# Kernel tuning notes

Hardware: AMD Instinct MI355X
Metric: run time of the kernel (lower is better)

The kernel has to match this reference:

```python
import jax, jax.numpy as jnp
import numpy as np

B, P, K = 8, 1024, 20  # clouds, points per cloud, kNN neighbors
OUT = 40
EPS = 1e-5


def leaky(x):
    return jnp.where(x >= 0, x, 0.2 * x)


def batch_norm(h, gamma, beta):
    mu = jnp.mean(h, axis=0)
    var = jnp.var(h, axis=0)
    return (h - mu) * jax.lax.rsqrt(var + EPS) * gamma + beta


def edge_conv(x, W, b, k):
    # x: [B,P,C]. Dynamic kNN in feature space (self included, as torch_cluster knn),
    # edge feature nn([x_i, x_j - x_i]) (single plain Linear per PyG MLP plain_last),
    # then max-aggregation over the k neighbors.
    sq = jnp.sum(x * x, axis=-1)                                  # [B,P]
    d = sq[:, :, None] + sq[:, None, :] - 2.0 * jnp.einsum('bpc,bqc->bpq', x, x)
    idx = jax.lax.top_k(-d, k)[1]                                  # [B,P,k]
    xj = jax.vmap(lambda xc, ic: xc[ic])(x, idx)                   # [B,P,k,C]
    xi = jnp.broadcast_to(x[:, :, None, :], xj.shape)
    e = jnp.concatenate([xi, xj - xi], axis=-1)                    # [B,P,k,2C]
    h = jnp.einsum('bpke,ec->bpkc', e, W) + b
    return jnp.max(h, axis=2)                                      # [B,P,Cout]


def setup_inputs() -> dict:
    key = jax.random.key(0)
    ks = jax.random.split(key, 16)
    s = 0.1
    pos = jax.random.normal(ks[0], (B * P, 3), dtype=jnp.float32)
    batch = jnp.repeat(jnp.arange(B, dtype=jnp.int32), P)
    return {
        'pos': pos, 'batch': batch,
        'W1': jax.random.normal(ks[1], (6, 64), jnp.float32) * s,    'b1': jnp.zeros((64,), jnp.float32),
        'W2': jax.random.normal(ks[2], (128, 64), jnp.float32) * s,  'b2': jnp.zeros((64,), jnp.float32),
        'W3': jax.random.normal(ks[3], (128, 128), jnp.float32) * s, 'b3': jnp.zeros((128,), jnp.float32),
        'W4': jax.random.normal(ks[4], (256, 256), jnp.float32) * s, 'b4': jnp.zeros((256,), jnp.float32),
        'Wm': jax.random.normal(ks[5], (512, 1024), jnp.float32) * s, 'bm': jnp.zeros((1024,), jnp.float32),
        'Wa': jax.random.normal(ks[6], (2048, 512), jnp.float32) * s, 'ba': jnp.zeros((512,), jnp.float32),
        'ga': jnp.ones((512,), jnp.float32),  'bea': jnp.zeros((512,), jnp.float32),
        'Wb': jax.random.normal(ks[7], (512, 256), jnp.float32) * s, 'bb': jnp.zeros((256,), jnp.float32),
        'gb': jnp.ones((256,), jnp.float32),  'beb': jnp.zeros((256,), jnp.float32),
        'Wc': jax.random.normal(ks[8], (256, OUT), jnp.float32) * s, 'bc': jnp.zeros((OUT,), jnp.float32),
    }


def reference(pos, batch, W1, b1, W2, b2, W3, b3, W4, b4, Wm, bm,
              Wa, ba, ga, bea, Wb, bb, gb, beb, Wc, bc):
    # batch ids are contiguous with P points per cloud -> reshape to [B,P,.]
    x = pos.reshape(B, P, 3)
    x1 = edge_conv(x, W1, b1, K)    # [B,P,64]
    x2 = edge_conv(x1, W2, b2, K)   # [B,P,64]
    x3 = edge_conv(x2, W3, b3, K)   # [B,P,128]
    x4 = edge_conv(x3, W4, b4, K)   # [B,P,256]
    cat = jnp.concatenate([x1, x2, x3, x4], axis=-1)  # [B,P,512]
    out = cat @ Wm + bm                                # [B,P,1024] (plain Linear)
    gmax = jnp.max(out, axis=1)                        # global_max_pool  [B,1024]
    gmean = jnp.mean(out, axis=1)                      # global_mean_pool [B,1024]
    h = jnp.concatenate([gmax, gmean], axis=-1)        # [B,2048]
    h = leaky(batch_norm(h @ Wa + ba, ga, bea))        # dropout = identity (eval)
    h = leaky(batch_norm(h @ Wb + bb, gb, beb))
    return h @ Wc + bc                                 # [B,40]
```

## Files before the change

### kernel.cpp

```cpp
#include <hip/hip_runtime.h>
#include <hip/hip_bf16.h>

#define NB 8
#define NP 1024
#define NPTS (NB * NP)
#define KNN 20

using bf16x8 = __attribute__((ext_vector_type(8))) short;
using f32x4 = __attribute__((ext_vector_type(4))) float;

static __device__ __forceinline__ unsigned long long umin64(unsigned long long a,
                                                            unsigned long long b) {
    return a < b ? a : b;
}

static __device__ __forceinline__ void split_bf16(float v, unsigned short& h,
                                                  unsigned short& l) {
    __hip_bfloat16 hb = __float2bfloat16(v);
    float hf = __bfloat162float(hb);
    __hip_bfloat16 lb = __float2bfloat16(v - hf);
    h = *(unsigned short*)&hb;
    l = *(unsigned short*)&lb;
}

static __device__ __forceinline__ unsigned long long wave_bitonic_sort(
        unsigned long long v, int lane) {
#pragma unroll
    for (int k = 2; k <= 64; k <<= 1) {
#pragma unroll
        for (int j = k >> 1; j > 0; j >>= 1) {
            unsigned long long o = __shfl_xor(v, j, 64);
            bool tmin = (((lane & k) == 0) == ((lane & j) == 0));
            bool lt = v < o;
            v = (lt == tmin) ? v : o;
        }
    }
    return v;
}

static __device__ __forceinline__ void topk20_wave(unsigned long long k[16], int lane,
                                                   int* __restrict__ out) {
    for (int r = 0; r < KNN; ++r) {
        unsigned long long m = k[0];
#pragma unroll
        for (int j = 1; j < 16; ++j)
            if ((unsigned)(k[j] >> 32) < (unsigned)(m >> 32)) m = k[j];
#pragma unroll
        for (int s = 1; s < 64; s <<= 1) {
            unsigned long long o = __shfl_xor(m, s, 64);
            m = umin64(m, o);
        }
        if (lane == 0) out[r] = (int)(m & 0xffffffffu);
        if (r == KNN - 1) break;
        unsigned mlo = (unsigned)m;
#pragma unroll
        for (int j = 0; j < 16; ++j)
            if ((unsigned)k[j] == mlo) k[j] = ~0ull;
    }
}

static __device__ __forceinline__ void topk20_fast(unsigned long long k[16], int lane,
                                                   unsigned long long* __restrict__ cand,
                                                   int* __restrict__ out) {
    unsigned long long lm = k[0];
#pragma unroll
    for (int j = 1; j < 16; ++j) lm = umin64(lm, k[j]);
    unsigned long long s = wave_bitonic_sort(lm, lane);
    unsigned long long T = __shfl(s, 19, 64);

    int base = 0;
#pragma unroll
    for (int j = 0; j < 16; ++j) {
        bool sel = (k[j] <= T);
        unsigned long long mask = __ballot(sel);
        if (sel) {
            int pos = base + (int)__popcll(mask & ((1ull << lane) - 1ull));
            if (pos < 64) cand[pos] = k[j];
        }
        base += (int)__popcll(mask);
    }
    if (base <= 64) {
        unsigned long long v = (lane < base) ? cand[lane] : ~0ull;
        v = wave_bitonic_sort(v, lane);
        if (lane < KNN) out[lane] = (int)(v & 0xffffffffu);
    } else {
        topk20_wave(k, lane, out);
    }
}

__global__ __launch_bounds__(256) void knn3_kernel(const float* __restrict__ x,
                                                   int* __restrict__ idx) {
    const int w = threadIdx.x >> 6, lane = threadIdx.x & 63;
    const int p = blockIdx.x * 4 + w;
    const int b = p >> 10, pr = p & 1023;
    const int tid = threadIdx.x;
    __shared__ float sx[3][1024];
    __shared__ float ssq[1024];
    __shared__ unsigned long long cand[4][64];
    const float* xb = x + (size_t)b * NP * 3;

    for (int t = tid; t < 1024; t += 256) {
        float vx = xb[t * 3 + 0], vy = xb[t * 3 + 1], vz = xb[t * 3 + 2];
        sx[0][t] = vx;
        sx[1][t] = vy;
        sx[2][t] = vz;
        ssq[t] = vx * vx + vy * vy + vz * vz;
    }
    __syncthreads();

    const float px = sx[0][pr], py = sx[1][pr], pz = sx[2][pr];
    const float sqp = ssq[pr];

    unsigned long long k[16];
#pragma unroll
    for (int j = 0; j < 16; ++j) {
        int q = j * 64 + lane;
        float dot = px * sx[0][q];
        dot += py * sx[1][q];
        dot += pz * sx[2][q];
        float d = sqp + ssq[q] - 2.0f * dot;
        unsigned u = __float_as_uint(d);
        u = (u & 0x80000000u) ? ~u : (u | 0x80000000u);
        k[j] = ((unsigned long long)u << 32) | (unsigned)q;
    }
    topk20_fast(k, lane, cand[w], idx + (size_t)p * KNN);
}

template <int C>
__global__ __launch_bounds__(256) void sqnorm_kernel(const float* __restrict__ x,
                                                     float* __restrict__ sqn) {
    int p = blockIdx.x * 256 + threadIdx.x;
    if (p < NPTS) {
        const float* xp = x + (size_t)p * C;
        float s = 0.f;
        for (int c = 0; c < C; ++c) s += xp[c] * xp[c];
        sqn[p] = s;
    }
}

template <int C>
__global__ __launch_bounds__(256) void convert_x_kernel(const float* __restrict__ x,
                                                        unsigned short* __restrict__ Xh,
                                                        unsigned short* __restrict__ Xl) {
    int g = blockIdx.x * 256 + threadIdx.x;
    int p = g & (NPTS - 1), ks = g >> 13;
    const float* src = x + (size_t)p * C + ks * 8;
    float4 v0 = ((const float4*)src)[0];
    float4 v1 = ((const float4*)src)[1];
    float v[8] = {v0.x, v0.y, v0.z, v0.w, v1.x, v1.y, v1.z, v1.w};
    unsigned short h[8], l[8];
#pragma unroll
    for (int j = 0; j < 8; ++j) split_bf16(v[j], h[j], l[j]);
    size_t ci = (size_t)ks * NPTS + p;
    uint4 hp, lp;
    hp.x = h[0] | ((unsigned)h[1] << 16);
    hp.y = h[2] | ((unsigned)h[3] << 16);
    hp.z = h[4] | ((unsigned)h[5] << 16);
    hp.w = h[6] | ((unsigned)h[7] << 16);
    lp.x = l[0] | ((unsigned)l[1] << 16);
    lp.y = l[2] | ((unsigned)l[3] << 16);
    lp.z = l[4] | ((unsigned)l[5] << 16);
    lp.w = l[6] | ((unsigned)l[7] << 16);
    ((uint4*)Xh)[ci] = hp;
    ((uint4*)Xl)[ci] = lp;
}

template <int Cin, int Cout>
__global__ __launch_bounds__(256) void convert_w_edge_kernel(
        const float* __restrict__ W, unsigned short* __restrict__ Wh,
        unsigned short* __restrict__ Wl) {
    constexpr int N2 = 2 * Cout;
    int g = blockIdx.x * 256 + threadIdx.x;
    if (g >= (Cin / 8) * N2) return;
    int n = g % N2, ks = g / N2;
    unsigned short h[8], l[8];
#pragma unroll
    for (int j = 0; j < 8; ++j) {
        int c = ks * 8 + j;
        float v;
        if (n < Cout)
            v = W[(size_t)c * Cout + n] - W[(size_t)(Cin + c) * Cout + n];
        else
            v = W[(size_t)(Cin + c) * Cout + (n - Cout)];
        split_bf16(v, h[j], l[j]);
    }
    size_t ci = (size_t)ks * N2 + n;
    uint4 hp, lp;
    hp.x = h[0] | ((unsigned)h[1] << 16);
    hp.y = h[2] | ((unsigned)h[3] << 16);
    hp.z = h[4] | ((unsigned)h[5] << 16);
    hp.w = h[6] | ((unsigned)h[7] << 16);
    lp.x = l[0] | ((unsigned)l[1] << 16);
    lp.y = l[2] | ((unsigned)l[3] << 16);
    lp.z = l[4] | ((unsigned)l[5] << 16);
    lp.w = l[6] | ((unsigned)l[7] << 16);
    ((uint4*)Wh)[ci] = hp;
    ((uint4*)Wl)[ci] = lp;
}

template <int C>
__global__ __launch_bounds__(256, 2) void knn_mfma_kernel(
        const unsigned short* __restrict__ Xhp, const unsigned short* __restrict__ Xlp,
        const float* __restrict__ sqn, int* __restrict__ idx) {
    constexpr int NCK = C / 32;
    const int bid = blockIdx.x;
    const int b = bid >> 6, rg = bid & 63;
    const int g0 = b * NP;
    const int p0 = rg * 16;
    const int tid = threadIdx.x;
    const int wid = tid >> 6, lane = tid & 63;
    const int fkb = lane >> 4, flm = lane & 15;

    __shared__ float sD[16][1028];
    __shared__ float sqa[16];
    __shared__ float sqb[1024];
    __shared__ unsigned long long cand[4][64];

    if (tid < 16) sqa[tid] = sqn[g0 + p0 + tid];
    for (int t = tid; t < 1024; t += 256) sqb[t] = sqn[g0 + t];
    __syncthreads();

    const uint4* Ah4 = (const uint4*)Xhp;
    const uint4* Al4 = (const uint4*)Xlp;

    uint4 fAh[NCK], fAl[NCK];
#pragma unroll
    for (int kk = 0; kk < NCK; ++kk) {
        size_t a = (size_t)(4 * kk + fkb) * NPTS + g0 + p0 + flm;
        fAh[kk] = Ah4[a];
        fAl[kk] = Al4[a];
    }

    const int r4 = fkb * 4, cc = flm;

#pragma unroll
    for (int t = 0; t < 2; ++t) {
        const int c0 = (wid + t * 4) * 128;
        f32x4 acc[8];
#pragma unroll
        for (int j = 0; j < 8; ++j) acc[j] = {0.f, 0.f, 0.f, 0.f};

#pragma unroll
        for (int kk = 0; kk < NCK; ++kk) {
            uint4 fBh[8], fBl[8];
#pragma unroll
            for (int j = 0; j < 8; ++j) {
                size_t bi = (size_t)(4 * kk + fkb) * NPTS + g0 + c0 + j * 16 + flm;
                fBh[j] = Ah4[bi];
                fBl[j] = Al4[bi];
            }
            bf16x8 ah = *(const bf16x8*)&fAh[kk];
            bf16x8 al = *(const bf16x8*)&fAl[kk];
#pragma unroll
            for (int j = 0; j < 8; ++j) {
                bf16x8 bh = *(const bf16x8*)&fBh[j];
                bf16x8 bl = *(const bf16x8*)&fBl[j];
                acc[j] = __builtin_amdgcn_mfma_f32_16x16x32_bf16(ah, bh, acc[j], 0, 0, 0);
                acc[j] = __builtin_amdgcn_mfma_f32_16x16x32_bf16(ah, bl, acc[j], 0, 0, 0);
                acc[j] = __builtin_amdgcn_mfma_f32_16x16x32_bf16(al, bh, acc[j], 0, 0, 0);
            }
        }

#pragma unroll
        for (int r = 0; r < 4; ++r) {
            int row = r4 + r;
            float sp = sqa[row];
#pragma unroll
            for (int j = 0; j < 8; ++j) {
                int col = c0 + j * 16 + cc;
                sD[row][col] = sp + sqb[col] - 2.0f * acc[j][r];
            }
        }
    }
    __syncthreads();

    for (int rr = 0; rr < 4; ++rr) {
        int row = wid * 4 + rr;
        unsigned long long k[16];
#pragma unroll
        for (int j = 0; j < 16; ++j) {
            int q = j * 64 + lane;
            float dv = sD[row][q];
            unsigned u = __float_as_uint(dv);
            u = (u & 0x80000000u) ? ~u : (u | 0x80000000u);
            k[j] = ((unsigned long long)u << 32) | (unsigned)q;
        }
        topk20_fast(k, lane, cand[wid], idx + (size_t)(g0 + p0 + row) * KNN);
        __builtin_amdgcn_s_barrier();
    }
}

template <int Cin, int Cout>
__global__ __launch_bounds__(256, 2) void edge_mfma_kernel(
        const unsigned short* __restrict__ Xhp, const unsigned short* __restrict__ Xlp,
        const unsigned short* __restrict__ Whp, const unsigned short* __restrict__ Wlp,
        const float* __restrict__ bias, float* __restrict__ AB) {
    constexpr int N2 = 2 * Cout;
    constexpr int NCK = Cin / 32;
    const int n0 = blockIdx.x * 128;
    const int p0 = blockIdx.y * 128;
    const int tid = threadIdx.x;
    const int wid = tid >> 6, lane = tid & 63;
    const int wm = (wid >> 1) * 64, wn = (wid & 1) * 64;

    __shared__ uint4 sAh[2][4][132], sAl[2][4][132], sBh[2][4][132], sBl[2][4][132];

    f32x4 acc[4][4];
#pragma unroll
    for (int i = 0; i < 4; ++i)
#pragma unroll
        for (int j = 0; j < 4; ++j) acc[i][j] = {0.f, 0.f, 0.f, 0.f};

    const uint4* Ah4 = (const uint4*)Xhp;
    const uint4* Al4 = (const uint4*)Xlp;
    const uint4* Wh4 = (const uint4*)Whp;
    const uint4* Wl4 = (const uint4*)Wlp;

    const int m0 = tid & 127, kb0 = tid >> 7;
    uint4 rAh0, rAl0, rBh0, rBl0, rAh1, rAl1, rBh1, rBl1;

#define EM_LOAD(ck)                                                     \
    {                                                                   \
        int ksb = (ck) * 4;                                             \
        size_t a0 = (size_t)(ksb + kb0) * NPTS + p0 + m0;               \
        size_t a1 = (size_t)(ksb + kb0 + 2) * NPTS + p0 + m0;           \
        size_t b0 = (size_t)(ksb + kb0) * N2 + n0 + m0;                 \
        size_t b1 = (size_t)(ksb + kb0 + 2) * N2 + n0 + m0;             \
        rAh0 = Ah4[a0]; rAl0 = Al4[a0];                                 \
        rAh1 = Ah4[a1]; rAl1 = Al4[a1];                                 \
        rBh0 = Wh4[b0]; rBl0 = Wl4[b0];                                 \
        rBh1 = Wh4[b1]; rBl1 = Wl4[b1];                                 \
    }

#define EM_WRITE(buf)                                                   \
    {                                                                   \
        sAh[buf][kb0][m0] = rAh0;  sAl[buf][kb0][m0] = rAl0;            \
        sAh[buf][kb0 + 2][m0] = rAh1;  sAl[buf][kb0 + 2][m0] = rAl1;    \
        sBh[buf][kb0][m0] = rBh0;  sBl[buf][kb0][m0] = rBl0;            \
        sBh[buf][kb0 + 2][m0] = rBh1;  sBl[buf][kb0 + 2][m0] = rBl1;    \
    }

    EM_LOAD(0);
    EM_WRITE(0);
    __syncthreads();

    const int fkb = lane >> 4, flm = lane & 15;

    for (int ck = 0; ck < NCK; ++ck) {
        const int buf = ck & 1;
        if (ck < NCK - 1) EM_LOAD(ck + 1);

        bf16x8 fAh[4], fAl[4], fBh[4], fBl[4];
#pragma unroll
        for (int i = 0; i < 4; ++i) {
            fAh[i] = *(const bf16x8*)&sAh[buf][fkb][wm + i * 16 + flm];
            fAl[i] = *(const bf16x8*)&sAl[buf][fkb][wm + i * 16 + flm];
            fBh[i] = *(const bf16x8*)&sBh[buf][fkb][wn + i * 16 + flm];
            fBl[i] = *(const bf16x8*)&sBl[buf][fkb][wn + i * 16 + flm];
        }
#pragma unroll
        for (int i = 0; i < 4; ++i)
#pragma unroll
            for (int j = 0; j < 4; ++j) {
                acc[i][j] = __builtin_amdgcn_mfma_f32_16x16x32_bf16(fAh[i], fBh[j],
                                                                    acc[i][j], 0, 0, 0);
                acc[i][j] = __builtin_amdgcn_mfma_f32_16x16x32_bf16(fAh[i], fBl[j],
                                                                    acc[i][j], 0, 0, 0);
                acc[i][j] = __builtin_amdgcn_mfma_f32_16x16x32_bf16(fAl[i], fBh[j],
                                                                    acc[i][j], 0, 0, 0);
            }

        if (ck < NCK - 1) EM_WRITE(buf ^ 1);
        __syncthreads();
    }

    const int r4 = (lane >> 4) * 4, cc = lane & 15;
    float bj[4];
#pragma unroll
    for (int j = 0; j < 4; ++j) {
        int cg = n0 + wn + j * 16 + cc;
        bj[j] = (cg < Cout) ? bias[cg] : 0.f;
    }
#pragma unroll
    for (int i = 0; i < 4; ++i) {
#pragma unroll
        for (int r = 0; r < 4; ++r) {
            int row = wm + i * 16 + r4 + r;
            float* orow = AB + (size_t)(p0 + row) * N2 + n0;
#pragma unroll
            for (int j = 0; j < 4; ++j)
                orow[wn + j * 16 + cc] = acc[i][j][r] + bj[j];
        }
    }
#undef EM_LOAD
#undef EM_WRITE
}

template <int Cin, int Cout>
__global__ __launch_bounds__(256) void edge_gemm_kernel(const float* __restrict__ x,
                                                        const float* __restrict__ W,
                                                        const float* __restrict__ bias,
                                                        float* __restrict__ AB) {
    constexpr int N2 = 2 * Cout;
    constexpr int BK = (Cin < 32) ? Cin : 32;
    const int n0 = blockIdx.x * 128;
    const int p0 = blockIdx.y * 64;
    const int tid = threadIdx.x;
    const int tx = tid & 15, ty = tid >> 4;

    __shared__ float sX[BK][68];
    __shared__ float sW[BK][132];

    float acc[4][8];
#pragma unroll
    for (int i = 0; i < 4; ++i)
#pragma unroll
        for (int j = 0; j < 8; ++j) acc[i][j] = 0.f;

    for (int k0 = 0; k0 < Cin; k0 += BK) {
        for (int t = tid; t < 64 * BK; t += 256) {
            int m = t / BK, c = t - m * BK;
            sX[c][m] = x[(size_t)(p0 + m) * Cin + c];
        }
        for (int t = tid; t < BK * 128; t += 256) {
            int c = t >> 7, n = t & 127;
            int nn = n0 + n;
            float w;
            if (nn < Cout)
                w = W[(size_t)(k0 + c) * Cout + nn] - W[(size_t)(Cin + k0 + c) * Cout + nn];
            else
                w = W[(size_t)(Cin + k0 + c) * Cout + (nn - Cout)];
            sW[c][n] = w;
        }
        __syncthreads();

#pragma unroll
        for (int c = 0; c < BK; ++c) {
            float4 a4 = *(const float4*)&sX[c][ty * 4];
            float4 w0 = *(const float4*)&sW[c][tx * 4];
            float4 w1 = *(const float4*)&sW[c][64 + tx * 4];
            float av[4] = {a4.x, a4.y, a4.z, a4.w};
#pragma unroll
            for (int i = 0; i < 4; ++i) {
                acc[i][0] += av[i] * w0.x;
                acc[i][1] += av[i] * w0.y;
                acc[i][2] += av[i] * w0.z;
                acc[i][3] += av[i] * w0.w;
                acc[i][4] += av[i] * w1.x;
                acc[i][5] += av[i] * w1.y;
                acc[i][6] += av[i] * w1.z;
                acc[i][7] += av[i] * w1.w;
            }
        }
        __syncthreads();
    }

    const bool aH0 = (n0 < Cout);
    const bool aH1 = (n0 + 64 < Cout);
    float4 z4 = {0.f, 0.f, 0.f, 0.f};
    float4 bb0 = aH0 ? *(const float4*)&bias[n0 + tx * 4] : z4;
    float4 bb1 = aH1 ? *(const float4*)&bias[n0 + 64 + tx * 4] : z4;

#pragma unroll
    for (int i = 0; i < 4; ++i) {
        float* orow = AB + (size_t)(p0 + ty * 4 + i) * N2 + n0;
        float4 o0, o1;
        o0.x = acc[i][0] + bb0.x;
        o0.y = acc[i][1] + bb0.y;
        o0.z = acc[i][2] + bb0.z;
        o0.w = acc[i][3] + bb0.w;
        o1.x = acc[i][4] + bb1.x;
        o1.y = acc[i][5] + bb1.y;
        o1.z = acc[i][6] + bb1.z;
        o1.w = acc[i][7] + bb1.w;
        *(float4*)&orow[tx * 4] = o0;
        *(float4*)&orow[64 + tx * 4] = o1;
    }
}

template <int Cout>
__global__ __launch_bounds__(256) void gather_max_kernel(const float* __restrict__ AB,
                                                         const int* __restrict__ idx,
                                                         float* __restrict__ y) {
    constexpr int N2 = 2 * Cout;
    constexpr int TPP = Cout / 4;
    constexpr int PPB = 256 / TPP;
    constexpr int RS = N2 / 4;
    const int pp = threadIdx.x / TPP;
    const int t = threadIdx.x % TPP;
    const int p = blockIdx.x * PPB + pp;
    const int base = p & ~(NP - 1);

    __shared__ int s_idx[PPB][KNN];
    for (int tt = threadIdx.x; tt < PPB * KNN; tt += 256) {
        int a = tt / KNN, r = tt - a * KNN;
        s_idx[a][r] = idx[(size_t)(blockIdx.x * PPB + a) * KNN + r];
    }
    __syncthreads();

    const float4* Brow = (const float4*)(AB + (size_t)base * N2 + Cout);

    int q0 = s_idx[pp][0];
    float4 m = Brow[(size_t)q0 * RS + t];
#pragma unroll
    for (int j = 1; j < KNN; ++j) {
        int q = s_idx[pp][j];
        float4 v = Brow[(size_t)q * RS + t];
        m.x = fmaxf(m.x, v.x);
        m.y = fmaxf(m.y, v.y);
        m.z = fmaxf(m.z, v.z);
        m.w = fmaxf(m.w, v.w);
    }
    float4 a = *(const float4*)(AB + (size_t)p * N2 + 4 * t);
    float4 o;
    o.x = a.x + m.x;
    o.y = a.y + m.y;
    o.z = a.z + m.z;
    o.w = a.w + m.w;
    *(float4*)(y + (size_t)p * Cout + 4 * t) = o;
}

__global__ __launch_bounds__(256) void convert_w_kernel(const float* __restrict__ Wm,
                                                        unsigned short* __restrict__ Wh,
                                                        unsigned short* __restrict__ Wl) {
    int g = blockIdx.x * 256 + threadIdx.x;
    int n = g & 1023, ks = g >> 10;
    unsigned short h[8], l[8];
#pragma unroll
    for (int j = 0; j < 8; ++j) {
        float v = Wm[(size_t)(ks * 8 + j) * 1024 + n];
        split_bf16(v, h[j], l[j]);
    }
    size_t ci = (size_t)ks * 1024 + n;
    uint4 hp, lp;
    hp.x = h[0] | ((unsigned)h[1] << 16);
    hp.y = h[2] | ((unsigned)h[3] << 16);
    hp.z = h[4] | ((unsigned)h[5] << 16);
    hp.w = h[6] | ((unsigned)h[7] << 16);
    lp.x = l[0] | ((unsigned)l[1] << 16);
    lp.y = l[2] | ((unsigned)l[3] << 16);
    lp.z = l[4] | ((unsigned)l[5] << 16);
    lp.w = l[6] | ((unsigned)l[7] << 16);
    ((uint4*)Wh)[ci] = hp;
    ((uint4*)Wl)[ci] = lp;
}

__global__ __launch_bounds__(256) void catmean_kernel(
        const float* __restrict__ x1, const float* __restrict__ x2,
        const float* __restrict__ x3, const float* __restrict__ x4,
        float* __restrict__ catmean) {
    const int n0 = blockIdx.x * 128;
    const int b = blockIdx.y;
    const int tid = threadIdx.x;
    const int col = n0 + (tid & 127);
    const int half = tid >> 7;
    __shared__ float sred[256];

    const float* src;
    int cw, coff;
    if (col < 64) { src = x1; cw = 64; coff = col; }
    else if (col < 128) { src = x2; cw = 64; coff = col - 64; }
    else if (col < 256) { src = x3; cw = 128; coff = col - 128; }
    else { src = x4; cw = 256; coff = col - 256; }

    float s = 0.f;
    const float* base = src + ((size_t)b * NP + half * 512) * cw + coff;
    for (int p = 0; p < 512; ++p) s += base[(size_t)p * cw];
    sred[tid] = s;
    __syncthreads();
    if (tid < 128)
        catmean[(size_t)b * 512 + col] = (sred[tid] + sred[tid + 128]) * (1.0f / 1024.0f);
}

__global__ __launch_bounds__(256) void gmean_kernel(const float* __restrict__ catmean,
                                                    const float* __restrict__ Wm,
                                                    const float* __restrict__ bm,
                                                    float* __restrict__ gmeanv) {
    const int n0 = blockIdx.x * 128;
    const int b = blockIdx.y;
    const int tid = threadIdx.x;
    const int cg = tid & 31, kp = tid >> 5;
    const int col = n0 + cg * 4;
    __shared__ float4 part[8][32];

    float4 acc = {0.f, 0.f, 0.f, 0.f};
    for (int k = kp * 64; k < kp * 64 + 64; ++k) {
        float g = catmean[(size_t)b * 512 + k];
        float4 w = *(const float4*)&Wm[(size_t)k * 1024 + col];
        acc.x += g * w.x;
        acc.y += g * w.y;
        acc.z += g * w.z;
        acc.w += g * w.w;
    }
    part[kp][cg] = acc;
    __syncthreads();
    if (tid < 32) {
        float4 s = part[0][tid];
#pragma unroll
        for (int z = 1; z < 8; ++z) {
            float4 p = part[z][tid];
            s.x += p.x; s.y += p.y; s.z += p.z; s.w += p.w;
        }
        float4 bb = *(const float4*)&bm[n0 + tid * 4];
        s.x += bb.x; s.y += bb.y; s.z += bb.z; s.w += bb.w;
        *(float4*)&gmeanv[(size_t)b * 1024 + n0 + tid * 4] = s;
    }
}

__global__ __launch_bounds__(256, 2) void gemm_cat_pool_kernel(
        const unsigned short* __restrict__ Ahp, const unsigned short* __restrict__ Alp,
        const unsigned short* __restrict__ Whp, const unsigned short* __restrict__ Wlp,
        float* __restrict__ pmax) {
    const int bid = blockIdx.x;
    const int xcd = bid & 7, pos = bid >> 3;
    const int nb = pos & 7, pb = (xcd << 3) | (pos >> 3);
    const int n0 = nb * 128, p0 = pb * 128;
    const int tid = threadIdx.x;
    const int wid = tid >> 6, lane = tid & 63;
    const int wm = (wid >> 1) * 64, wn = (wid & 1) * 64;

    __shared__ uint4 sAh[2][4][132], sAl[2][4][132], sBh[2][4][132], sBl[2][4][132];
    __shared__ float sMax[2][128];

    f32x4 acc[4][4];
#pragma unroll
    for (int i = 0; i < 4; ++i)
#pragma unroll
        for (int j = 0; j < 4; ++j) acc[i][j] = {0.f, 0.f, 0.f, 0.f};

    const uint4* Ah4 = (const uint4*)Ahp;
    const uint4* Al4 = (const uint4*)Alp;
    const uint4* Wh4 = (const uint4*)Whp;
    const uint4* Wl4 = (const uint4*)Wlp;

    const int m0 = tid & 127, kb0 = tid >> 7;
    uint4 rAh0, rAl0, rBh0, rBl0, rAh1, rAl1, rBh1, rBl1;

#define MP_LOAD(ck)                                                     \
    {                                                                   \
        int ksb = (ck) * 4;                                             \
        size_t a0 = (size_t)(ksb + kb0) * 8192 + p0 + m0;               \
        size_t a1 = (size_t)(ksb + kb0 + 2) * 8192 + p0 + m0;           \
        size_t b0 = (size_t)(ksb + kb0) * 1024 + n0 + m0;               \
        size_t b1 = (size_t)(ksb + kb0 + 2) * 1024 + n0 + m0;           \
        rAh0 = Ah4[a0]; rAl0 = Al4[a0];                                 \
        rAh1 = Ah4[a1]; rAl1 = Al4[a1];                                 \
        rBh0 = Wh4[b0]; rBl0 = Wl4[b0];                                 \
        rBh1 = Wh4[b1]; rBl1 = Wl4[b1];                                 \
    }

#define MP_WRITE(buf)                                                   \
    {                                                                   \
        sAh[buf][kb0][m0] = rAh0;  sAl[buf][kb0][m0] = rAl0;            \
        sAh[buf][kb0 + 2][m0] = rAh1;  sAl[buf][kb0 + 2][m0] = rAl1;    \
        sBh[buf][kb0][m0] = rBh0;  sBl[buf][kb0][m0] = rBl0;            \
        sBh[buf][kb0 + 2][m0] = rBh1;  sBl[buf][kb0 + 2][m0] = rBl1;    \
    }

    MP_LOAD(0);
    MP_WRITE(0);
    __syncthreads();

    const int fkb = lane >> 4, flm = lane & 15;

    for (int ck = 0; ck < 16; ++ck) {
        const int buf = ck & 1;
        if (ck < 15) MP_LOAD(ck + 1);

        bf16x8 fAh[4], fAl[4], fBh[4], fBl[4];
#pragma unroll
        for (int i = 0; i < 4; ++i) {
            fAh[i] = *(const bf16x8*)&sAh[buf][fkb][wm + i * 16 + flm];
            fAl[i] = *(const bf16x8*)&sAl[buf][fkb][wm + i * 16 + flm];
            fBh[i] = *(const bf16x8*)&sBh[buf][fkb][wn + i * 16 + flm];
            fBl[i] = *(const bf16x8*)&sBl[buf][fkb][wn + i * 16 + flm];
        }
#pragma unroll
        for (int i = 0; i < 4; ++i)
#pragma unroll
            for (int j = 0; j < 4; ++j) {
                acc[i][j] = __builtin_amdgcn_mfma_f32_16x16x32_bf16(fAh[i], fBh[j],
                                                                    acc[i][j], 0, 0, 0);
                acc[i][j] = __builtin_amdgcn_mfma_f32_16x16x32_bf16(fAh[i], fBl[j],
                                                                    acc[i][j], 0, 0, 0);
                acc[i][j] = __builtin_amdgcn_mfma_f32_16x16x32_bf16(fAl[i], fBh[j],
                                                                    acc[i][j], 0, 0, 0);
            }

        if (ck < 15) MP_WRITE(buf ^ 1);
        __syncthreads();
    }

    float cm[4];
#pragma unroll
    for (int j = 0; j < 4; ++j) {
        float m = acc[0][j][0];
#pragma unroll
        for (int i = 0; i < 4; ++i)
#pragma unroll
            for (int r = 0; r < 4; ++r) m = fmaxf(m, acc[i][j][r]);
        m = fmaxf(m, __shfl_xor(m, 16, 64));
        m = fmaxf(m, __shfl_xor(m, 32, 64));
        cm[j] = m;
    }
    if (lane < 16) {
#pragma unroll
        for (int j = 0; j < 4; ++j) sMax[wid >> 1][wn + j * 16 + lane] = cm[j];
    }
    __syncthreads();
    if (tid < 128)
        pmax[(size_t)pb * 1024 + n0 + tid] = fmaxf(sMax[0][tid], sMax[1][tid]);
#undef MP_LOAD
#undef MP_WRITE
}

__global__ __launch_bounds__(256) void fc_a_kernel(const float* __restrict__ pmax,
                                                   const float* __restrict__ gmeanv,
                                                   const float* __restrict__ bm,
                                                   const float* __restrict__ Wa,
                                                   const float* __restrict__ ba,
                                                   float* __restrict__ ha) {
    const int b = blockIdx.y;
    const int n0 = blockIdx.x * 64;
    const int tid = threadIdx.x;
    __shared__ float gm[2048];
    __shared__ float4 part[16][16];

    for (int c = tid; c < 1024; c += 256) {
        float m = pmax[(size_t)(b * 8) * 1024 + c];
#pragma unroll
        for (int z = 1; z < 8; ++z) m = fmaxf(m, pmax[(size_t)(b * 8 + z) * 1024 + c]);
        gm[c] = m + bm[c];
        gm[1024 + c] = gmeanv[(size_t)b * 1024 + c];
    }
    __syncthreads();

    const int cg = tid & 15, kp = tid >> 4;
    const int co = n0 + cg * 4;
    float4 acc = {0.f, 0.f, 0.f, 0.f};
    const float* Wp = Wa + (size_t)(kp * 128) * 512 + co;
    const float* gp = gm + kp * 128;
#pragma unroll 8
    for (int k = 0; k < 128; ++k) {
        float g = gp[k];
        float4 w = *(const float4*)&Wp[(size_t)k * 512];
        acc.x += g * w.x;
        acc.y += g * w.y;
        acc.z += g * w.z;
        acc.w += g * w.w;
    }
    part[kp][cg] = acc;
    __syncthreads();
    if (tid < 16) {
        float4 s = part[0][tid];
#pragma unroll
        for (int z = 1; z < 16; ++z) {
            float4 p = part[z][tid];
            s.x += p.x; s.y += p.y; s.z += p.z; s.w += p.w;
        }
        float4 bb = *(const float4*)&ba[n0 + tid * 4];
        s.x += bb.x; s.y += bb.y; s.z += bb.z; s.w += bb.w;
        *(float4*)&ha[(size_t)b * 512 + n0 + tid * 4] = s;
    }
}

__global__ __launch_bounds__(256) void bn_leaky_kernel(float* __restrict__ h,
                                                       const float* __restrict__ g,
                                                       const float* __restrict__ be,
                                                       int ncol) {
    int co = blockIdx.x * 256 + threadIdx.x;
    if (co >= ncol) return;
    float mu = 0.f;
    for (int b = 0; b < NB; ++b) mu += h[b * ncol + co];
    mu *= 0.125f;
    float var = 0.f;
    for (int b = 0; b < NB; ++b) {
        float d = h[b * ncol + co] - mu;
        var += d * d;
    }
    var *= 0.125f;
    float inv = 1.0f / sqrtf(var + 1e-5f);
    for (int b = 0; b < NB; ++b) {
        float v = (h[b * ncol + co] - mu) * inv * g[co] + be[co];
        h[b * ncol + co] = v >= 0.f ? v : 0.2f * v;
    }
}

__global__ __launch_bounds__(256) void fc_b_kernel(const float* __restrict__ ha,
                                                   const float* __restrict__ Wb,
                                                   const float* __restrict__ bb,
                                                   float* __restrict__ hb) {
    const int b = blockIdx.y;
    const int n0 = blockIdx.x * 64;
    const int tid = threadIdx.x;
    __shared__ float sh[512];
    __shared__ float4 part[16][16];

    for (int c = tid; c < 512; c += 256) sh[c] = ha[(size_t)b * 512 + c];
    __syncthreads();

    const int cg = tid & 15, kp = tid >> 4;
    const int co = n0 + cg * 4;
    float4 acc = {0.f, 0.f, 0.f, 0.f};
#pragma unroll 8
    for (int k = 0; k < 32; ++k) {
        float g = sh[kp * 32 + k];
        float4 w = *(const float4*)&Wb[(size_t)(kp * 32 + k) * 256 + co];
        acc.x += g * w.x;
        acc.y += g * w.y;
        acc.z += g * w.z;
        acc.w += g * w.w;
    }
    part[kp][cg] = acc;
    __syncthreads();
    if (tid < 16) {
        float4 s = part[0][tid];
#pragma unroll
        for (int z = 1; z < 16; ++z) {
            float4 p = part[z][tid];
            s.x += p.x; s.y += p.y; s.z += p.z; s.w += p.w;
        }
        float4 bv = *(const float4*)&bb[n0 + tid * 4];
        s.x += bv.x; s.y += bv.y; s.z += bv.z; s.w += bv.w;
        *(float4*)&hb[(size_t)b * 256 + n0 + tid * 4] = s;
    }
}

__global__ __launch_bounds__(256) void fc_c_kernel(const float* __restrict__ hb,
                                                   const float* __restrict__ Wc,
                                                   const float* __restrict__ bc,
                                                   float* __restrict__ outp) {
    int t = blockIdx.x * 256 + threadIdx.x;
    if (t >= 8 * 40) return;
    int b = t / 40, o = t - b * 40;
    float s = bc[o];
    for (int c = 0; c < 256; ++c) s += hb[b * 256 + c] * Wc[c * 40 + o];
    outp[t] = s;
}

extern "C" void kernel_launch(void* const* d_in, const int* in_sizes, int n_in,
                              void* d_out, int out_size, void* d_ws, size_t ws_size,
                              hipStream_t stream) {
    const float* pos = (const float*)d_in[0];
    const float* W1 = (const float*)d_in[2];
    const float* b1 = (const float*)d_in[3];
    const float* W2 = (const float*)d_in[4];
    const float* b2 = (const float*)d_in[5];
    const float* W3 = (const float*)d_in[6];
    const float* b3 = (const float*)d_in[7];
    const float* W4 = (const float*)d_in[8];
    const float* b4 = (const float*)d_in[9];
    const float* Wm = (const float*)d_in[10];
    const float* bm = (const float*)d_in[11];
    const float* Wa = (const float*)d_in[12];
    const float* ba = (const float*)d_in[13];
    const float* ga = (const float*)d_in[14];
    const float* bea = (const float*)d_in[15];
    const float* Wb = (const float*)d_in[16];
    const float* bb = (const float*)d_in[17];
    const float* gb = (const float*)d_in[18];
    const float* beb = (const float*)d_in[19];
    const float* Wc = (const float*)d_in[20];
    const float* bc = (const float*)d_in[21];
    float* out = (float*)d_out;

    char* ws = (char*)d_ws;
    size_t off = 0;
    auto alloc = [&](size_t bytes) {
        void* p = ws + off;
        off += (bytes + 255) & ~(size_t)255;
        return p;
    };
    int* idx = (int*)alloc((size_t)NPTS * KNN * 4);
    float* x1 = (float*)alloc((size_t)NPTS * 64 * 4);
    float* x2 = (float*)alloc((size_t)NPTS * 64 * 4);
    float* x3 = (float*)alloc((size_t)NPTS * 128 * 4);
    float* x4 = (float*)alloc((size_t)NPTS * 256 * 4);
    float* scratch = (float*)alloc((size_t)NPTS * 512 * 4);
    float* pmax = (float*)alloc((size_t)64 * 1024 * 4);
    float* catmean = (float*)alloc(NB * 512 * 4);
    float* gmeanv = (float*)alloc(NB * 1024 * 4);
    float* ha = (float*)alloc(NB * 512 * 4);
    float* hb = (float*)alloc(NB * 256 * 4);
    float* sqn = (float*)alloc(NPTS * 4);
    unsigned short* Ach = (unsigned short*)alloc((size_t)64 * NPTS * 8 * 2);
    unsigned short* Acl = (unsigned short*)alloc((size_t)64 * NPTS * 8 * 2);
    unsigned short* Wth = (unsigned short*)alloc((size_t)64 * 1024 * 8 * 2);
    unsigned short* Wtl = (unsigned short*)alloc((size_t)64 * 1024 * 8 * 2);
    unsigned short* Weh = (unsigned short*)alloc((size_t)16 * 512 * 8 * 2);
    unsigned short* Wel = (unsigned short*)alloc((size_t)16 * 512 * 8 * 2);
    (void)ws_size;

    float* AB = scratch;
    const size_t REG = (size_t)NPTS * 8;
    unsigned short* x1h = Ach, *x1l = Acl;
    unsigned short* x2h = Ach + 8 * REG, *x2l = Acl + 8 * REG;
    unsigned short* x3h = Ach + 16 * REG, *x3l = Acl + 16 * REG;
    unsigned short* x4h = Ach + 32 * REG, *x4l = Acl + 32 * REG;

    knn3_kernel<<<NPTS / 4, 256, 0, stream>>>(pos, idx);
    edge_gemm_kernel<3, 64><<<dim3(1, 128), 256, 0, stream>>>(pos, W1, b1, AB);
    gather_max_kernel<64><<<NPTS / 16, 256, 0, stream>>>(AB, idx, x1);

    convert_x_kernel<64><<<NPTS * 8 / 256, 256, 0, stream>>>(x1, x1h, x1l);
    sqnorm_kernel<64><<<NPTS / 256, 256, 0, stream>>>(x1, sqn);
    knn_mfma_kernel<64><<<512, 256, 0, stream>>>(x1h, x1l, sqn, idx);
    convert_w_edge_kernel<64, 64><<<4, 256, 0, stream>>>(W2, Weh, Wel);
    edge_mfma_kernel<64, 64><<<dim3(1, 64), 256, 0, stream>>>(x1h, x1l, Weh, Wel, b2, AB);
    gather_max_kernel<64><<<NPTS / 16, 256, 0, stream>>>(AB, idx, x2);

    convert_x_kernel<64><<<NPTS * 8 / 256, 256, 0, stream>>>(x2, x2h, x2l);
    sqnorm_kernel<64><<<NPTS / 256, 256, 0, stream>>>(x2, sqn);
    knn_mfma_kernel<64><<<512, 256, 0, stream>>>(x2h, x2l, sqn, idx);
    convert_w_edge_kernel<64, 128><<<8, 256, 0, stream>>>(W3, Weh, Wel);
    edge_mfma_kernel<64, 128><<<dim3(2, 64), 256, 0, stream>>>(x2h, x2l, Weh, Wel, b3, AB);
    gather_max_kernel<128><<<NPTS / 8, 256, 0, stream>>>(AB, idx, x3);

    convert_x_kernel<128><<<NPTS * 16 / 256, 256, 0, stream>>>(x3, x3h, x3l);
    sqnorm_kernel<128><<<NPTS / 256, 256, 0, stream>>>(x3, sqn);
    knn_mfma_kernel<128><<<512, 256, 0, stream>>>(x3h, x3l, sqn, idx);
    convert_w_edge_kernel<128, 256><<<32, 256, 0, stream>>>(W4, Weh, Wel);
    edge_mfma_kernel<128, 256><<<dim3(4, 64), 256, 0, stream>>>(x3h, x3l, Weh, Wel, b4, AB);
    gather_max_kernel<256><<<NPTS / 4, 256, 0, stream>>>(AB, idx, x4);

    convert_x_kernel<256><<<NPTS * 32 / 256, 256, 0, stream>>>(x4, x4h, x4l);

    catmean_kernel<<<dim3(4, NB), 256, 0, stream>>>(x1, x2, x3, x4, catmean);
    gmean_kernel<<<dim3(8, NB), 256, 0, stream>>>(catmean, Wm, bm, gmeanv);

    convert_w_kernel<<<256, 256, 0, stream>>>(Wm, Wth, Wtl);

    gemm_cat_pool_kernel<<<512, 256, 0, stream>>>(Ach, Acl, Wth, Wtl, pmax);

    fc_a_kernel<<<dim3(8, NB), 256, 0, stream>>>(pmax, gmeanv, bm, Wa, ba, ha);
    bn_leaky_kernel<<<2, 256, 0, stream>>>(ha, ga, bea, 512);
    fc_b_kernel<<<dim3(4, NB), 256, 0, stream>>>(ha, Wb, bb, hb);
    bn_leaky_kernel<<<1, 256, 0, stream>>>(hb, gb, beb, 256);
    fc_c_kernel<<<2, 256, 0, stream>>>(hb, Wc, bc, out);
}
```

Measured before the change: 268.9 us.

## Fuse bf16 split into gather-max, batch weight conversions, fuse BN into FC kernels

Converting activations to hi/lo bf16 panels now happens in the gather-max epilogue, which removes four separate convert_x passes. All weight conversions are merged into one kernel launched up front, and each edge layer gets its own weight buffer. Batch norm plus leaky ReLU is folded into the following FC kernels, and a per-row barrier in the kNN top-k loop is dropped. The goal is fewer kernel launches and less global memory traffic, at the cost of redundant BN computation per block and some risk from removing the barrier.

```diff
diff --git a/kernel.cpp b/kernel.cpp
--- a/kernel.cpp
+++ b/kernel.cpp
@@ -138,53 +138,10 @@
     }
 }
 
-template <int C>
-__global__ __launch_bounds__(256) void convert_x_kernel(const float* __restrict__ x,
-                                                        unsigned short* __restrict__ Xh,
-                                                        unsigned short* __restrict__ Xl) {
-    int g = blockIdx.x * 256 + threadIdx.x;
-    int p = g & (NPTS - 1), ks = g >> 13;
-    const float* src = x + (size_t)p * C + ks * 8;
-    float4 v0 = ((const float4*)src)[0];
-    float4 v1 = ((const float4*)src)[1];
-    float v[8] = {v0.x, v0.y, v0.z, v0.w, v1.x, v1.y, v1.z, v1.w};
-    unsigned short h[8], l[8];
-#pragma unroll
-    for (int j = 0; j < 8; ++j) split_bf16(v[j], h[j], l[j]);
-    size_t ci = (size_t)ks * NPTS + p;
-    uint4 hp, lp;
-    hp.x = h[0] | ((unsigned)h[1] << 16);
-    hp.y = h[2] | ((unsigned)h[3] << 16);
-    hp.z = h[4] | ((unsigned)h[5] << 16);
-    hp.w = h[6] | ((unsigned)h[7] << 16);
-    lp.x = l[0] | ((unsigned)l[1] << 16);
-    lp.y = l[2] | ((unsigned)l[3] << 16);
-    lp.z = l[4] | ((unsigned)l[5] << 16);
-    lp.w = l[6] | ((unsigned)l[7] << 16);
-    ((uint4*)Xh)[ci] = hp;
-    ((uint4*)Xl)[ci] = lp;
-}
-
-template <int Cin, int Cout>
-__global__ __launch_bounds__(256) void convert_w_edge_kernel(
-        const float* __restrict__ W, unsigned short* __restrict__ Wh,
-        unsigned short* __restrict__ Wl) {
-    constexpr int N2 = 2 * Cout;
-    int g = blockIdx.x * 256 + threadIdx.x;
-    if (g >= (Cin / 8) * N2) return;
-    int n = g % N2, ks = g / N2;
-    unsigned short h[8], l[8];
-#pragma unroll
-    for (int j = 0; j < 8; ++j) {
-        int c = ks * 8 + j;
-        float v;
-        if (n < Cout)
-            v = W[(size_t)c * Cout + n] - W[(size_t)(Cin + c) * Cout + n];
-        else
-            v = W[(size_t)(Cin + c) * Cout + (n - Cout)];
-        split_bf16(v, h[j], l[j]);
-    }
-    size_t ci = (size_t)ks * N2 + n;
+static __device__ __forceinline__ void pack_store(unsigned short h[8],
+                                                  unsigned short l[8], size_t ci,
+                                                  unsigned short* __restrict__ Wh,
+                                                  unsigned short* __restrict__ Wl) {
     uint4 hp, lp;
     hp.x = h[0] | ((unsigned)h[1] << 16);
     hp.y = h[2] | ((unsigned)h[3] << 16);
@@ -196,6 +153,53 @@
     lp.w = l[6] | ((unsigned)l[7] << 16);
     ((uint4*)Wh)[ci] = hp;
     ((uint4*)Wl)[ci] = lp;
+}
+
+static __device__ void conv_edge_w(const float* __restrict__ W, int Cin, int Cout,
+                                   int g, unsigned short* __restrict__ Wh,
+                                   unsigned short* __restrict__ Wl) {
+    int N2 = 2 * Cout;
+    if (g >= (Cin / 8) * N2) return;
+    int n = g % N2, ks = g / N2;
+    unsigned short h[8], l[8];
+#pragma unroll
+    for (int j = 0; j < 8; ++j) {
+        int c = ks * 8 + j;
+        float v;
+        if (n < Cout)
+            v = W[(size_t)c * Cout + n] - W[(size_t)(Cin + c) * Cout + n];
+        else
+            v = W[(size_t)(Cin + c) * Cout + (n - Cout)];
+        split_bf16(v, h[j], l[j]);
+    }
+    pack_store(h, l, (size_t)ks * N2 + n, Wh, Wl);
+}
+
+__global__ __launch_bounds__(256) void convert_all_w_kernel(
+        const float* __restrict__ Wm, const float* __restrict__ W2,
+        const float* __restrict__ W3, const float* __restrict__ W4,
+        unsigned short* __restrict__ Wmh, unsigned short* __restrict__ Wml,
+        unsigned short* __restrict__ W2h, unsigned short* __restrict__ W2l,
+        unsigned short* __restrict__ W3h, unsigned short* __restrict__ W3l,
+        unsigned short* __restrict__ W4h, unsigned short* __restrict__ W4l) {
+    int bid = blockIdx.x;
+    if (bid < 256) {
+        int g = bid * 256 + threadIdx.x;
+        int n = g & 1023, ks = g >> 10;
+        unsigned short h[8], l[8];
+#pragma unroll
+        for (int j = 0; j < 8; ++j) {
+            float v = Wm[(size_t)(ks * 8 + j) * 1024 + n];
+            split_bf16(v, h[j], l[j]);
+        }
+        pack_store(h, l, (size_t)ks * 1024 + n, Wmh, Wml);
+    } else if (bid < 288) {
+        conv_edge_w(W4, 128, 256, (bid - 256) * 256 + threadIdx.x, W4h, W4l);
+    } else if (bid < 296) {
+        conv_edge_w(W3, 64, 128, (bid - 288) * 256 + threadIdx.x, W3h, W3l);
+    } else {
+        conv_edge_w(W2, 64, 64, (bid - 296) * 256 + threadIdx.x, W2h, W2l);
+    }
 }
 
 template <int C>
@@ -286,7 +290,6 @@
             k[j] = ((unsigned long long)u << 32) | (unsigned)q;
         }
         topk20_fast(k, lane, cand[wid], idx + (size_t)(g0 + p0 + row) * KNN);
-        __builtin_amdgcn_s_barrier();
     }
 }
 
@@ -479,9 +482,10 @@
 }
 
 template <int Cout>
-__global__ __launch_bounds__(256) void gather_max_kernel(const float* __restrict__ AB,
-                                                         const int* __restrict__ idx,
-                                                         float* __restrict__ y) {
+__global__ __launch_bounds__(256) void gather_max_panel_kernel(
+        const float* __restrict__ AB, const int* __restrict__ idx,
+        float* __restrict__ y, unsigned short* __restrict__ Xh,
+        unsigned short* __restrict__ Xl) {
     constexpr int N2 = 2 * Cout;
     constexpr int TPP = Cout / 4;
     constexpr int PPB = 256 / TPP;
@@ -518,31 +522,21 @@
     o.z = a.z + m.z;
     o.w = a.w + m.w;
     *(float4*)(y + (size_t)p * Cout + 4 * t) = o;
-}
-
-__global__ __launch_bounds__(256) void convert_w_kernel(const float* __restrict__ Wm,
-                                                        unsigned short* __restrict__ Wh,
-                                                        unsigned short* __restrict__ Wl) {
-    int g = blockIdx.x * 256 + threadIdx.x;
-    int n = g & 1023, ks = g >> 10;
-    unsigned short h[8], l[8];
-#pragma unroll
-    for (int j = 0; j < 8; ++j) {
-        float v = Wm[(size_t)(ks * 8 + j) * 1024 + n];
-        split_bf16(v, h[j], l[j]);
-    }
-    size_t ci = (size_t)ks * 1024 + n;
-    uint4 hp, lp;
+
+    unsigned short h[4], l[4];
+    split_bf16(o.x, h[0], l[0]);
+    split_bf16(o.y, h[1], l[1]);
+    split_bf16(o.z, h[2], l[2]);
+    split_bf16(o.w, h[3], l[3]);
+    const int ks = t >> 1;
+    size_t u2 = ((size_t)ks * NPTS + p) * 2 + (t & 1);
+    uint2 hp, lp;
     hp.x = h[0] | ((unsigned)h[1] << 16);
     hp.y = h[2] | ((unsigned)h[3] << 16);
-    hp.z = h[4] | ((unsigned)h[5] << 16);
-    hp.w = h[6] | ((unsigned)h[7] << 16);
     lp.x = l[0] | ((unsigned)l[1] << 16);
     lp.y = l[2] | ((unsigned)l[3] << 16);
-    lp.z = l[4] | ((unsigned)l[5] << 16);
-    lp.w = l[6] | ((unsigned)l[7] << 16);
-    ((uint4*)Wh)[ci] = hp;
-    ((uint4*)Wl)[ci] = lp;
+    ((uint2*)Xh)[u2] = hp;
+    ((uint2*)Xl)[u2] = lp;
 }
 
 __global__ __launch_bounds__(256) void catmean_kernel(
@@ -764,39 +758,36 @@
     }
 }
 
-__global__ __launch_bounds__(256) void bn_leaky_kernel(float* __restrict__ h,
-                                                       const float* __restrict__ g,
-                                                       const float* __restrict__ be,
-                                                       int ncol) {
-    int co = blockIdx.x * 256 + threadIdx.x;
-    if (co >= ncol) return;
-    float mu = 0.f;
-    for (int b = 0; b < NB; ++b) mu += h[b * ncol + co];
-    mu *= 0.125f;
-    float var = 0.f;
-    for (int b = 0; b < NB; ++b) {
-        float d = h[b * ncol + co] - mu;
-        var += d * d;
-    }
-    var *= 0.125f;
-    float inv = 1.0f / sqrtf(var + 1e-5f);
-    for (int b = 0; b < NB; ++b) {
-        float v = (h[b * ncol + co] - mu) * inv * g[co] + be[co];
-        h[b * ncol + co] = v >= 0.f ? v : 0.2f * v;
-    }
-}
-
-__global__ __launch_bounds__(256) void fc_b_kernel(const float* __restrict__ ha,
-                                                   const float* __restrict__ Wb,
-                                                   const float* __restrict__ bb,
-                                                   float* __restrict__ hb) {
+__global__ __launch_bounds__(256) void fc_b_bn_kernel(const float* __restrict__ ha,
+                                                      const float* __restrict__ g,
+                                                      const float* __restrict__ be,
+                                                      const float* __restrict__ Wb,
+                                                      const float* __restrict__ bb,
+                                                      float* __restrict__ hb) {
     const int b = blockIdx.y;
     const int n0 = blockIdx.x * 64;
     const int tid = threadIdx.x;
+    __shared__ float shall[NB][512];
     __shared__ float sh[512];
     __shared__ float4 part[16][16];
 
-    for (int c = tid; c < 512; c += 256) sh[c] = ha[(size_t)b * 512 + c];
+    for (int t = tid; t < NB * 512; t += 256) shall[t >> 9][t & 511] = ha[t];
+    __syncthreads();
+
+    for (int c = tid; c < 512; c += 256) {
+        float mu = 0.f;
+        for (int z = 0; z < NB; ++z) mu += shall[z][c];
+        mu *= 0.125f;
+        float var = 0.f;
+        for (int z = 0; z < NB; ++z) {
+            float d = shall[z][c] - mu;
+            var += d * d;
+        }
+        var *= 0.125f;
+        float inv = 1.0f / sqrtf(var + 1e-5f);
+        float v = (shall[b][c] - mu) * inv * g[c] + be[c];
+        sh[c] = v >= 0.f ? v : 0.2f * v;
+    }
     __syncthreads();
 
     const int cg = tid & 15, kp = tid >> 4;
@@ -804,12 +795,12 @@
     float4 acc = {0.f, 0.f, 0.f, 0.f};
 #pragma unroll 8
     for (int k = 0; k < 32; ++k) {
-        float g = sh[kp * 32 + k];
+        float gg = sh[kp * 32 + k];
         float4 w = *(const float4*)&Wb[(size_t)(kp * 32 + k) * 256 + co];
-        acc.x += g * w.x;
-        acc.y += g * w.y;
-        acc.z += g * w.z;
-        acc.w += g * w.w;
+        acc.x += gg * w.x;
+        acc.y += gg * w.y;
+        acc.z += gg * w.z;
+        acc.w += gg * w.w;
     }
     part[kp][cg] = acc;
     __syncthreads();
@@ -826,16 +817,47 @@
     }
 }
 
-__global__ __launch_bounds__(256) void fc_c_kernel(const float* __restrict__ hb,
-                                                   const float* __restrict__ Wc,
-                                                   const float* __restrict__ bc,
-                                                   float* __restrict__ outp) {
-    int t = blockIdx.x * 256 + threadIdx.x;
-    if (t >= 8 * 40) return;
-    int b = t / 40, o = t - b * 40;
-    float s = bc[o];
-    for (int c = 0; c < 256; ++c) s += hb[b * 256 + c] * Wc[c * 40 + o];
-    outp[t] = s;
+__global__ __launch_bounds__(256) void fc_c_bn_kernel(const float* __restrict__ hbin,
+                                                      const float* __restrict__ g,
+                                                      const float* __restrict__ be,
+                                                      const float* __restrict__ Wc,
+                                                      const float* __restrict__ bc,
+                                                      float* __restrict__ outp) {
+    const int tid = threadIdx.x;
+    __shared__ float shn[NB][256];
+
+    {
+        int c = tid;
+        float col[NB];
+#pragma unroll
+        for (int z = 0; z < NB; ++z) col[z] = hbin[z * 256 + c];
+        float mu = 0.f;
+#pragma unroll
+        for (int z = 0; z < NB; ++z) mu += col[z];
+        mu *= 0.125f;
+        float var = 0.f;
+#pragma unroll
+        for (int z = 0; z < NB; ++z) {
+            float d = col[z] - mu;
+            var += d * d;
+        }
+        var *= 0.125f;
+        float inv = 1.0f / sqrtf(var + 1e-5f);
+#pragma unroll
+        for (int z = 0; z < NB; ++z) {
+            float v = (col[z] - mu) * inv * g[c] + be[c];
+            shn[z][c] = v >= 0.f ? v : 0.2f * v;
+        }
+    }
+    __syncthreads();
+
+    int t = blockIdx.x * 256 + tid;
+    if (t < 8 * 40) {
+        int b = t / 40, o = t - b * 40;
+        float s = bc[o];
+        for (int c = 0; c < 256; ++c) s += shn[b][c] * Wc[c * 40 + o];
+        outp[t] = s;
+    }
 }
 
 extern "C" void kernel_launch(void* const* d_in, const int* in_sizes, int n_in,
@@ -887,8 +909,12 @@
     unsigned short* Acl = (unsigned short*)alloc((size_t)64 * NPTS * 8 * 2);
     unsigned short* Wth = (unsigned short*)alloc((size_t)64 * 1024 * 8 * 2);
     unsigned short* Wtl = (unsigned short*)alloc((size_t)64 * 1024 * 8 * 2);
-    unsigned short* Weh = (unsigned short*)alloc((size_t)16 * 512 * 8 * 2);
-    unsigned short* Wel = (unsigned short*)alloc((size_t)16 * 512 * 8 * 2);
+    unsigned short* W2h = (unsigned short*)alloc((size_t)8 * 128 * 8 * 2);
+    unsigned short* W2l = (unsigned short*)alloc((size_t)8 * 128 * 8 * 2);
+    unsigned short* W3h = (unsigned short*)alloc((size_t)8 * 256 * 8 * 2);
+    unsigned short* W3l = (unsigned short*)alloc((size_t)8 * 256 * 8 * 2);
+    unsigned short* W4h = (unsigned short*)alloc((size_t)16 * 512 * 8 * 2);
+    unsigned short* W4l = (unsigned short*)alloc((size_t)16 * 512 * 8 * 2);
     (void)ws_size;
 
     float* AB = scratch;
@@ -898,43 +924,34 @@
     unsigned short* x3h = Ach + 16 * REG, *x3l = Acl + 16 * REG;
     unsigned short* x4h = Ach + 32 * REG, *x4l = Acl + 32 * REG;
 
+    convert_all_w_kernel<<<300, 256, 0, stream>>>(Wm, W2, W3, W4, Wth, Wtl, W2h, W2l,
+                                                  W3h, W3l, W4h, W4l);
+
     knn3_kernel<<<NPTS / 4, 256, 0, stream>>>(pos, idx);
     edge_gemm_kernel<3, 64><<<dim3(1, 128), 256, 0, stream>>>(pos, W1, b1, AB);
-    gather_max_kernel<64><<<NPTS / 16, 256, 0, stream>>>(AB, idx, x1);
-
-    convert_x_kernel<64><<<NPTS * 8 / 256, 256, 0, stream>>>(x1, x1h, x1l);
+    gather_max_panel_kernel<64><<<NPTS / 16, 256, 0, stream>>>(AB, idx, x1, x1h, x1l);
+
     sqnorm_kernel<64><<<NPTS / 256, 256, 0, stream>>>(x1, sqn);
     knn_mfma_kernel<64><<<512, 256, 0, stream>>>(x1h, x1l, sqn, idx);
-    convert_w_edge_kernel<64, 64><<<4, 256, 0, stream>>>(W2, Weh, Wel);
-    edge_mfma_kernel<64, 64><<<dim3(1, 64), 256, 0, stream>>>(x1h, x1l, Weh, Wel, b2, AB);
-    gather_max_kernel<64><<<NPTS / 16, 256, 0, stream>>>(AB, idx, x2);
-
-    convert_x_kernel<64><<<NPTS * 8 / 256, 256, 0, stream>>>(x2, x2h, x2l);
+    edge_mfma_kernel<64, 64><<<dim3(1, 64), 256, 0, stream>>>(x1h, x1l, W2h, W2l, b2, AB);
+    gather_max_panel_kernel<64><<<NPTS / 16, 256, 0, stream>>>(AB, idx, x2, x2h, x2l);
+
     sqnorm_kernel<64><<<NPTS / 256, 256, 0, stream>>>(x2, sqn);
     knn_mfma_kernel<64><<<512, 256, 0, stream>>>(x2h, x2l, sqn, idx);
-    convert_w_edge_kernel<64, 128><<<8, 256, 0, stream>>>(W3, Weh, Wel);
-    edge_mfma_kernel<64, 128><<<dim3(2, 64), 256, 0, stream>>>(x2h, x2l, Weh, Wel, b3, AB);
-    gather_max_kernel<128><<<NPTS / 8, 256, 0, stream>>>(AB, idx, x3);
-
-    convert_x_kernel<128><<<NPTS * 16 / 256, 256, 0, stream>>>(x3, x3h, x3l);
+    edge_mfma_kernel<64, 128><<<dim3(2, 64), 256, 0, stream>>>(x2h, x2l, W3h, W3l, b3, AB);
+    gather_max_panel_kernel<128><<<NPTS / 8, 256, 0, stream>>>(AB, idx, x3, x3h, x3l);
+
     sqnorm_kernel<128><<<NPTS / 256, 256, 0, stream>>>(x3, sqn);
     knn_mfma_kernel<128><<<512, 256, 0, stream>>>(x3h, x3l, sqn, idx);
-    convert_w_edge_kernel<128, 256><<<32, 256, 0, stream>>>(W4, Weh, Wel);
-    edge_mfma_kernel<128, 256><<<dim3(4, 64), 256, 0, stream>>>(x3h, x3l, Weh, Wel, b4, AB);
-    gather_max_kernel<256><<<NPTS / 4, 256, 0, stream>>>(AB, idx, x4);
-
-    convert_x_kernel<256><<<NPTS * 32 / 256, 256, 0, stream>>>(x4, x4h, x4l);
+    edge_mfma_kernel<128, 256><<<dim3(4, 64), 256, 0, stream>>>(x3h, x3l, W4h, W4l, b4, AB);
+    gather_max_panel_kernel<256><<<NPTS / 4, 256, 0, stream>>>(AB, idx, x4, x4h, x4l);
 
     catmean_kernel<<<dim3(4, NB), 256, 0, stream>>>(x1, x2, x3, x4, catmean);
     gmean_kernel<<<dim3(8, NB), 256, 0, stream>>>(catmean, Wm, bm, gmeanv);
 
-    convert_w_kernel<<<256, 256, 0, stream>>>(Wm, Wth, Wtl);
-
     gemm_cat_pool_kernel<<<512, 256, 0, stream>>>(Ach, Acl, Wth, Wtl, pmax);
 
     fc_a_kernel<<<dim3(8, NB), 256, 0, stream>>>(pmax, gmeanv, bm, Wa, ba, ha);
-    bn_leaky_kernel<<<2, 256, 0, stream>>>(ha, ga, bea, 512);
-    fc_b_kernel<<<dim3(4, NB), 256, 0, stream>>>(ha, Wb, bb, hb);
-    bn_leaky_kernel<<<1, 256, 0, stream>>>(hb, gb, beb, 256);
-    fc_c_kernel<<<2, 256, 0, stream>>>(hb, Wc, bc, out);
-}
+    fc_b_bn_kernel<<<dim3(4, NB), 256, 0, stream>>>(ha, ga, bea, Wb, bb, hb);
+    fc_c_bn_kernel<<<2, 256, 0, stream>>>(hb, gb, beb, Wc, bc, out);
+}
```

After: 252.1 us. -6.2%, faster.
